# Optimization experiments

Hardware: AMD Instinct MI355X
Metric: run time of the kernel (lower is better)

## Reference

```python
import jax, jax.numpy as jnp
import numpy as np

N_LAYERS = 2        # f_aux_layer_num
DIM = 512           # aux_dim
HEADS = 8           # aux_attn_num
HEAD = DIM // HEADS # 64 == aux_attn_dim
FFN_H = int(DIM * 2.0)  # ffn_factor = 2.0 -> 1024
BLOCK = 64          # f_block_size n
L_BLOCKS = 32
M = BLOCK + 1       # block + router token
EPS = 1e-5
THETA = 10000.0


def rms_norm(x, w):
    return x * jax.lax.rsqrt(jnp.mean(x * x, axis=-1, keepdims=True) + EPS) * w


def rotary(x):
    # x: [b, h, s, a]; matches RotaryEmb: halves rotated with outer(t, inv_freq)
    s, a = x.shape[2], x.shape[3]
    inv_freq = (1.0 / THETA) ** (jnp.arange(0, a, 2, dtype=jnp.float32) / a)
    freqs = jnp.arange(s, dtype=jnp.float32)[:, None] * inv_freq[None, :]  # [s, a/2]
    cos, sin = jnp.cos(freqs), jnp.sin(freqs)
    x1, x2 = jnp.split(x, 2, axis=-1)
    return jnp.concatenate([x1 * cos + x2 * sin, -x1 * sin + x2 * cos], axis=-1)


def setup_inputs() -> dict:
    key = jax.random.key(0)
    ks = jax.random.split(key, 10)
    B = 2
    S = L_BLOCKS * M
    x = jax.random.normal(ks[0], (B, L_BLOCKS * BLOCK, DIM), jnp.float32)
    doc = jnp.sort(jax.random.randint(ks[1], (B, S), 0, 4, dtype=jnp.int32), axis=-1)
    w = 0.02
    return {
        "x": x,
        "doc": doc,
        "router_token": jax.random.normal(ks[2], (DIM,), jnp.float32),
        "attn_w": jax.random.normal(ks[3], (N_LAYERS, DIM, 3 * DIM), jnp.float32) * w,
        "attn_o_w": jax.random.normal(ks[4], (N_LAYERS, DIM, DIM), jnp.float32) * w,
        "ffn_up_w": jax.random.normal(ks[5], (N_LAYERS, DIM, 2 * FFN_H), jnp.float32) * w,
        "ffn_down_w": jax.random.normal(ks[6], (N_LAYERS, FFN_H, DIM), jnp.float32) * w,
        "attn_norm_w": jnp.ones((N_LAYERS, DIM), jnp.float32),
        "ffn_norm_w": jnp.ones((N_LAYERS, DIM), jnp.float32),
    }


def reference(x, doc, router_token, attn_w, attn_o_w, ffn_up_w, ffn_down_w,
              attn_norm_w, ffn_norm_w):
    b = x.shape[0]
    # insert router token after each block: [b, l, n+1, d] -> [b, s, d]
    xb = x.reshape(b, L_BLOCKS, BLOCK, DIM)
    rt = jnp.broadcast_to(router_token, (b, L_BLOCKS, 1, DIM))
    h = jnp.concatenate([xb, rt], axis=2).reshape(b, L_BLOCKS * M, DIM)
    s = h.shape[1]

    # mask_mod_1: block-causal AND same-doc
    blk = jnp.arange(s) // M
    causal = blk[:, None] >= blk[None, :]                       # [s, s]
    mask = causal[None] & (doc[:, :, None] == doc[:, None, :])  # [b, s, s]
    neg = jnp.finfo(h.dtype).min
    scale = 1.0 / jnp.sqrt(jnp.float32(HEAD))

    def split_heads(t):
        return t.reshape(b, s, HEADS, HEAD).transpose(0, 2, 1, 3)

    for i in range(N_LAYERS):
        hn = rms_norm(h, attn_norm_w[i])
        qkv = hn @ attn_w[i]                       # [b, s, 3*dim]
        q, k, v = jnp.split(qkv, 3, axis=-1)
        q, k, v = split_heads(q), split_heads(k), split_heads(v)
        q, k = rotary(q), rotary(k)
        scores = jnp.einsum('bhqa,bhka->bhqk', q, k) * scale
        scores = jnp.where(mask[:, None], scores, neg)
        attn = jax.nn.softmax(scores, axis=-1)
        o = jnp.einsum('bhqk,bhka->bhqa', attn, v)
        o = o.transpose(0, 2, 1, 3).reshape(b, s, DIM)
        h = h + o @ attn_o_w[i]
        hf = rms_norm(h, ffn_norm_w[i])
        u1, u2 = jnp.split(hf @ ffn_up_w[i], 2, axis=-1)
        h = h + (jax.nn.silu(u1) * u2) @ ffn_down_w[i]

    # keep router-token slot of each block: [b, l, d]
    return h.reshape(b, L_BLOCKS, M, DIM)[:, :, -1]
```

## Files before the change

kernel.cpp:

```cpp
#include <hip/hip_runtime.h>
#include <math.h>

#define NB 2
#define LB 32
#define BLKN 64
#define MM 65
#define SS (LB*MM)
#define DD 512
#define NH 8
#define HD 64
#define FFH 1024
#define ROWS (NB*SS)
#define WT_LS 2621440

typedef __attribute__((ext_vector_type(8))) short bf16x8;
typedef __attribute__((ext_vector_type(4))) float f32x4;

__device__ __forceinline__ unsigned short f2bf(float f) {
    union { float f; unsigned u; } v; v.f = f;
    unsigned r = (v.u + 0x7FFFu + ((v.u >> 16) & 1u)) >> 16;
    return (unsigned short)r;
}
__device__ __forceinline__ float bf2f(unsigned short u) {
    union { unsigned u; float f; } v; v.u = ((unsigned)u) << 16; return v.f;
}

__device__ __forceinline__ void gload_lds16(const unsigned short* g, unsigned short* l) {
    __builtin_amdgcn_global_load_lds((const __attribute__((address_space(1))) unsigned int*)g,
                                     (__attribute__((address_space(3))) unsigned int*)l,
                                     16, 0, 0);
}

__device__ __forceinline__ int grow_map(int r) {
    return (r >> 5) * SS + (r & 31) * MM + BLKN;
}

template <int FIRST>
__global__ __launch_bounds__(256) void rms4_k(const float* __restrict__ hsrc,
                                              const float* __restrict__ x,
                                              const float* __restrict__ rt,
                                              const float* __restrict__ w,
                                              float* __restrict__ hout,
                                              unsigned short* __restrict__ out) {
    int row = blockIdx.x * 4 + (threadIdx.x >> 6);
    int lane = threadIdx.x & 63;
    const float* sp;
    if (FIRST) {
        int s = row % SS, b = row / SS;
        int l = s / MM, j = s % MM;
        sp = (j < BLKN) ? x + ((size_t)(b * LB + l) * BLKN + j) * DD : rt;
    } else {
        sp = hsrc + (size_t)row * DD;
    }
    float4 a = *(const float4*)(sp + lane * 8);
    float4 bq = *(const float4*)(sp + lane * 8 + 4);
    float ss = a.x * a.x + a.y * a.y + a.z * a.z + a.w * a.w
             + bq.x * bq.x + bq.y * bq.y + bq.z * bq.z + bq.w * bq.w;
    #pragma unroll
    for (int off = 32; off; off >>= 1) ss += __shfl_xor(ss, off);
    float r = rsqrtf(ss * (1.0f / 512.0f) + 1e-5f);
    float4 w0 = *(const float4*)(w + lane * 8);
    float4 w1 = *(const float4*)(w + lane * 8 + 4);
    unsigned short o8[8] = {f2bf(a.x * r * w0.x), f2bf(a.y * r * w0.y),
                            f2bf(a.z * r * w0.z), f2bf(a.w * r * w0.w),
                            f2bf(bq.x * r * w1.x), f2bf(bq.y * r * w1.y),
                            f2bf(bq.z * r * w1.z), f2bf(bq.w * r * w1.w)};
    *(bf16x8*)(out + (size_t)row * DD + lane * 8) = *(const bf16x8*)o8;
    if (FIRST) {
        *(float4*)(hout + (size_t)row * DD + lane * 8) = a;
        *(float4*)(hout + (size_t)row * DD + lane * 8 + 4) = bq;
    }
}

__global__ __launch_bounds__(256) void wtrans_all_k(const float* __restrict__ attn_w,
                                                    const float* __restrict__ attn_o_w,
                                                    const float* __restrict__ up_w,
                                                    const float* __restrict__ down_w,
                                                    unsigned short* __restrict__ wt) {
    __shared__ unsigned short T[64][66];
    int wg = blockIdx.x;
    int layer = wg >= 640;
    int r = wg - layer * 640;
    const float* W; int K, N; size_t dstOff; int perm = 0;
    if (r < 192)      { W = attn_w   + (size_t)layer * 512 * 1536; K = 512;  N = 1536; dstOff = 0; }
    else if (r < 256) { W = attn_o_w + (size_t)layer * 512 * 512;  K = 512;  N = 512;  dstOff = 786432;  r -= 192; }
    else if (r < 512) { W = up_w     + (size_t)layer * 512 * 2048; K = 512;  N = 2048; dstOff = 1048576; perm = 1; r -= 256; }
    else              { W = down_w   + (size_t)layer * 1024 * 512; K = 1024; N = 512;  dstOff = 2097152; r -= 512; }
    unsigned short* dst = wt + (size_t)layer * WT_LS + dstOff;
    int ntn = N >> 6;
    int n0 = (r % ntn) * 64, k0 = (r / ntn) * 64;
    int t = threadIdx.x;
    #pragma unroll
    for (int i = 0; i < 16; ++i) {
        int e = t + i * 256;
        int rr = e >> 6, cc = e & 63;
        T[rr][cc] = f2bf(W[(size_t)(k0 + rr) * N + n0 + cc]);
    }
    __syncthreads();
    #pragma unroll
    for (int i = 0; i < 16; ++i) {
        int e = t + i * 256;
        int rr = e >> 6, cc = e & 63;
        int n = n0 + rr;
        int nr = n;
        if (perm) {
            int p = n & 1023;
            nr = ((p >> 4) << 5) | ((n >> 10) << 4) | (p & 15);
        }
        dst[(size_t)nr * K + k0 + cc] = T[cc][rr];
    }
}

template <int ADD, int OBF, int ROPE, int SILU>
__global__ __launch_bounds__(256) void gemm128_k(const unsigned short* __restrict__ A,
                                                 const unsigned short* __restrict__ Wt,
                                                 void* __restrict__ Cp,
                                                 int K, int N, int colOff) {
    __shared__ unsigned short As[128 * 64];
    __shared__ unsigned short Bs[128 * 64];
    int t = threadIdx.x;
    int lane = t & 63, wv = t >> 6;
    int wm = wv >> 1, wn = wv & 1;
    int rowBase = blockIdx.y * 128, colBase = blockIdx.x * 128;
    int c = lane & 15, g = lane >> 4;
    int sw = (c & 7) << 4;

    f32x4 acc[4][4];
    #pragma unroll
    for (int mt = 0; mt < 4; ++mt)
        #pragma unroll
        for (int nt = 0; nt < 4; ++nt) { f32x4 z = {0, 0, 0, 0}; acc[mt][nt] = z; }

    for (int k0 = 0; k0 < K; k0 += 64) {
        __syncthreads();
        #pragma unroll
        for (int i = 0; i < 4; ++i) {
            int e0 = (i * 4 + wv) * 64;
            int e = e0 + lane;
            int row = e >> 3;
            int kb = ((e & 7) << 4) ^ ((row & 7) << 4);
            int gr = rowBase + row; if (gr > ROWS - 1) gr = ROWS - 1;
            gload_lds16(A + (size_t)gr * K + k0 + (kb >> 1), &As[e0 * 8]);
        }
        #pragma unroll
        for (int i = 0; i < 4; ++i) {
            int e0 = (i * 4 + wv) * 64;
            int e = e0 + lane;
            int row = e >> 3;
            int kb = ((e & 7) << 4) ^ ((row & 7) << 4);
            gload_lds16(Wt + (size_t)(colOff + colBase + row) * K + k0 + (kb >> 1), &Bs[e0 * 8]);
        }
        __syncthreads();

        bf16x8 af[4][2], bfr[4][2];
        #pragma unroll
        for (int mt = 0; mt < 4; ++mt)
            #pragma unroll
            for (int hf = 0; hf < 2; ++hf)
                af[mt][hf] = *(const bf16x8*)
                    &As[((wm * 64 + mt * 16 + c) * 128 + ((hf * 64 + g * 16) ^ sw)) >> 1];
        #pragma unroll
        for (int nt = 0; nt < 4; ++nt)
            #pragma unroll
            for (int hf = 0; hf < 2; ++hf)
                bfr[nt][hf] = *(const bf16x8*)
                    &Bs[((wn * 64 + nt * 16 + c) * 128 + ((hf * 64 + g * 16) ^ sw)) >> 1];
        __builtin_amdgcn_s_setprio(1);
        #pragma unroll
        for (int mt = 0; mt < 4; ++mt)
            #pragma unroll
            for (int nt = 0; nt < 4; ++nt) {
                acc[mt][nt] = __builtin_amdgcn_mfma_f32_16x16x32_bf16(af[mt][0], bfr[nt][0], acc[mt][nt], 0, 0, 0);
                acc[mt][nt] = __builtin_amdgcn_mfma_f32_16x16x32_bf16(af[mt][1], bfr[nt][1], acc[mt][nt], 0, 0, 0);
            }
        __builtin_amdgcn_s_setprio(0);
    }

    if (ROPE) {
        int sec = (colOff + colBase + wn * 64) >> 9;
        if (sec < 2) {
            #pragma unroll
            for (int mt = 0; mt < 4; ++mt)
                #pragma unroll
                for (int j = 0; j < 4; ++j) {
                    int row = rowBase + wm * 64 + mt * 16 + g * 4 + j;
                    int spos = row % SS;
                    #pragma unroll
                    for (int p = 0; p < 2; ++p) {
                        float jj = (float)(c + p * 16);
                        float inv = exp2f(jj * -0.41524101186092030f);
                        float fr = (float)spos * inv;
                        float sn, cs; __sincosf(fr, &sn, &cs);
                        float a = acc[mt][p][j], bb = acc[mt][p + 2][j];
                        acc[mt][p][j] = a * cs + bb * sn;
                        acc[mt][p + 2][j] = -a * sn + bb * cs;
                    }
                }
        }
    }

    #pragma unroll
    for (int mt = 0; mt < 4; ++mt)
        #pragma unroll
        for (int j = 0; j < 4; ++j) {
            int row = rowBase + wm * 64 + mt * 16 + g * 4 + j;
            if (row >= ROWS) continue;
            if (SILU) {
                unsigned short* gr = (unsigned short*)Cp + (size_t)row * 1024;
                #pragma unroll
                for (int ntp = 0; ntp < 2; ++ntp) {
                    int npr = colBase + wn * 64 + ntp * 32;
                    int p = ((npr >> 5) << 4) + c;
                    float u1 = acc[mt][2 * ntp][j];
                    float u2 = acc[mt][2 * ntp + 1][j];
                    gr[p] = f2bf((u1 / (1.0f + __expf(-u1))) * u2);
                }
            } else {
                size_t off = (size_t)row * N + colOff + colBase + wn * 64 + c;
                if (OBF) {
                    unsigned short* cr = (unsigned short*)Cp + off;
                    #pragma unroll
                    for (int nt = 0; nt < 4; ++nt) cr[nt * 16] = f2bf(acc[mt][nt][j]);
                } else {
                    float* cr = (float*)Cp + off;
                    #pragma unroll
                    for (int nt = 0; nt < 4; ++nt) {
                        if (ADD) cr[nt * 16] += acc[mt][nt][j];
                        else     cr[nt * 16] = acc[mt][nt][j];
                    }
                }
            }
        }
}

template <int MODE, int ADD>
__global__ __launch_bounds__(256) void gemm64_k(const unsigned short* __restrict__ A,
                                                const unsigned short* __restrict__ Wt,
                                                void* __restrict__ Cp,
                                                const float* __restrict__ Hsrc,
                                                float* __restrict__ outp,
                                                int K, int N) {
    __shared__ unsigned short As[64 * 64];
    __shared__ unsigned short Bs[128 * 64];
    int t = threadIdx.x;
    int lane = t & 63, wv = t >> 6;
    int wm = wv >> 1, wn = wv & 1;
    int rowBase = blockIdx.y * 64, colBase = blockIdx.x * 128;
    int c = lane & 15, g = lane >> 4;
    int sw = (c & 7) << 4;

    f32x4 acc[2][4];
    #pragma unroll
    for (int mt = 0; mt < 2; ++mt)
        #pragma unroll
        for (int nt = 0; nt < 4; ++nt) { f32x4 z = {0, 0, 0, 0}; acc[mt][nt] = z; }

    for (int k0 = 0; k0 < K; k0 += 64) {
        __syncthreads();
        #pragma unroll
        for (int i = 0; i < 2; ++i) {
            int e0 = (i * 4 + wv) * 64;
            int e = e0 + lane;
            int row = e >> 3;
            int kb = ((e & 7) << 4) ^ ((row & 7) << 4);
            int gr = rowBase + row;
            if (MODE == 1) gr = grow_map(gr);
            gload_lds16(A + (size_t)gr * K + k0 + (kb >> 1), &As[e0 * 8]);
        }
        #pragma unroll
        for (int i = 0; i < 4; ++i) {
            int e0 = (i * 4 + wv) * 64;
            int e = e0 + lane;
            int row = e >> 3;
            int kb = ((e & 7) << 4) ^ ((row & 7) << 4);
            gload_lds16(Wt + (size_t)(colBase + row) * K + k0 + (kb >> 1), &Bs[e0 * 8]);
        }
        __syncthreads();

        bf16x8 af[2][2], bfr[4][2];
        #pragma unroll
        for (int mt = 0; mt < 2; ++mt)
            #pragma unroll
            for (int hf = 0; hf < 2; ++hf)
                af[mt][hf] = *(const bf16x8*)
                    &As[((wm * 32 + mt * 16 + c) * 128 + ((hf * 64 + g * 16) ^ sw)) >> 1];
        #pragma unroll
        for (int nt = 0; nt < 4; ++nt)
            #pragma unroll
            for (int hf = 0; hf < 2; ++hf)
                bfr[nt][hf] = *(const bf16x8*)
                    &Bs[((wn * 64 + nt * 16 + c) * 128 + ((hf * 64 + g * 16) ^ sw)) >> 1];
        __builtin_amdgcn_s_setprio(1);
        #pragma unroll
        for (int mt = 0; mt < 2; ++mt)
            #pragma unroll
            for (int nt = 0; nt < 4; ++nt) {
                acc[mt][nt] = __builtin_amdgcn_mfma_f32_16x16x32_bf16(af[mt][0], bfr[nt][0], acc[mt][nt], 0, 0, 0);
                acc[mt][nt] = __builtin_amdgcn_mfma_f32_16x16x32_bf16(af[mt][1], bfr[nt][1], acc[mt][nt], 0, 0, 0);
            }
        __builtin_amdgcn_s_setprio(0);
    }

    #pragma unroll
    for (int mt = 0; mt < 2; ++mt)
        #pragma unroll
        for (int j = 0; j < 4; ++j) {
            int row = rowBase + wm * 32 + mt * 16 + g * 4 + j;
            int col = colBase + wn * 64 + c;
            if (MODE == 0) {
                float* cr = (float*)Cp + (size_t)row * N + col;
                #pragma unroll
                for (int nt = 0; nt < 4; ++nt) {
                    if (ADD) cr[nt * 16] += acc[mt][nt][j];
                    else     cr[nt * 16] = acc[mt][nt][j];
                }
            } else if (MODE == 1) {
                int gr = grow_map(row);
                int spos = gr % SS;
                #pragma unroll
                for (int p = 0; p < 2; ++p) {
                    float jj = (float)(c + p * 16);
                    float inv = exp2f(jj * -0.41524101186092030f);
                    float fr = (float)spos * inv;
                    float sn, cs; __sincosf(fr, &sn, &cs);
                    float a = acc[mt][p][j], bb = acc[mt][p + 2][j];
                    acc[mt][p][j] = a * cs + bb * sn;
                    acc[mt][p + 2][j] = -a * sn + bb * cs;
                }
                unsigned short* cr = (unsigned short*)Cp + (size_t)gr * 1536 + col;
                #pragma unroll
                for (int nt = 0; nt < 4; ++nt) cr[nt * 16] = f2bf(acc[mt][nt][j]);
            } else if (MODE == 2) {
                int gr = grow_map(row);
                float* cr = (float*)Cp + (size_t)row * 512 + col;
                const float* hsr = Hsrc + (size_t)gr * 512 + col;
                #pragma unroll
                for (int nt = 0; nt < 4; ++nt) cr[nt * 16] = hsr[nt * 16] + acc[mt][nt][j];
            } else if (MODE == 3) {
                float* cr = outp + (size_t)row * 512 + col;
                const float* hsr = Hsrc + (size_t)row * 512 + col;
                #pragma unroll
                for (int nt = 0; nt < 4; ++nt) cr[nt * 16] = hsr[nt * 16] + acc[mt][nt][j];
            } else {
                unsigned short* gr = (unsigned short*)Cp + (size_t)row * 1024;
                #pragma unroll
                for (int ntp = 0; ntp < 2; ++ntp) {
                    int npr = colBase + wn * 64 + ntp * 32;
                    int p = ((npr >> 5) << 4) + c;
                    float u1 = acc[mt][2 * ntp][j];
                    float u2 = acc[mt][2 * ntp + 1][j];
                    gr[p] = f2bf((u1 / (1.0f + __expf(-u1))) * u2);
                }
            }
        }
}

#define QR 80

template <int ROUTER>
__global__ __launch_bounds__(320) void attn_mfma_k(const unsigned short* __restrict__ qkv,
                                                   const int* __restrict__ doc,
                                                   unsigned short* __restrict__ o,
                                                   unsigned short* __restrict__ obr) {
    __shared__ unsigned short Qs[QR * 64];
    __shared__ unsigned short Ks[2][64 * 64];
    __shared__ unsigned short Vt[2][64][72];
    __shared__ unsigned short Ps[5][16][72];
    __shared__ int docq[QR];
    __shared__ int dock[2][64];

    int idx = blockIdx.x;
    int l = 31 - (idx >> 4);
    int b = (idx >> 3) & 1;
    int h = idx & 7;
    int t = threadIdx.x;
    int lane = t & 63;
    int wv = t >> 6;

    const unsigned short* qb = qkv + (size_t)b * SS * 1536;
    int rowq0 = l * MM;
    int kmax = (l + 1) * MM;

    #pragma unroll
    for (int it = 0; it < 2; ++it) {
        int ebase = it * 320 + wv * 64;
        int e = ebase + lane;
        int row = e >> 3;
        int kb = ((e & 7) << 4) ^ ((row & 7) << 4);
        int gr = rowq0 + row; if (gr > SS - 1) gr = SS - 1;
        gload_lds16(qb + (size_t)gr * 1536 + h * 64 + (kb >> 1), &Qs[ebase * 8]);
    }
    if (t < QR) docq[t] = (t < MM) ? doc[b * SS + rowq0 + t] : -999999;

    int d0 = doc[b * SS + rowq0 + (ROUTER ? BLKN : 0)];
    int lo = 0, hi = rowq0;
    while (lo < hi) {
        int mid = (lo + hi) >> 1;
        if (doc[b * SS + mid] < d0) lo = mid + 1; else hi = mid;
    }
    int kts = lo >> 6;
    int nkt = (kmax + 63) >> 6;

    const int mt = wv;
    const int g = lane >> 4;
    const int c = lane & 15;
    const int sw = (c & 7) << 4;
    const bool act = ROUTER ? (wv == 4) : true;

    auto stageK = [&](int kbase, int buf) {
        int ebase = wv * 64;
        int e = ebase + lane;
        int row = e >> 3;
        int kb = ((e & 7) << 4) ^ ((row & 7) << 4);
        int kg = kbase + row; if (kg > kmax - 1) kg = kmax - 1;
        gload_lds16(qb + (size_t)kg * 1536 + 512 + h * 64 + (kb >> 1), &Ks[buf][ebase * 8]);
        if (wv < 3) {
            int eb2 = 320 + wv * 64;
            int e2 = eb2 + lane;
            int row2 = e2 >> 3;
            int kb2 = ((e2 & 7) << 4) ^ ((row2 & 7) << 4);
            int kg2 = kbase + row2; if (kg2 > kmax - 1) kg2 = kmax - 1;
            gload_lds16(qb + (size_t)kg2 * 1536 + 512 + h * 64 + (kb2 >> 1), &Ks[buf][eb2 * 8]);
        }
    };
    bf16x8 vr0, vr1; int dnx = 0;
    auto loadV = [&](int kbase) {
        int key = t & 63;
        int de = (t >> 6) * 8;
        int kg = kbase + key; if (kg > kmax - 1) kg = kmax - 1;
        vr0 = *(const bf16x8*)(qb + (size_t)kg * 1536 + 1024 + h * 64 + de);
        if (t < 192) {
            int e2 = 320 + t;
            int key2 = e2 & 63;
            int de2 = (e2 >> 6) * 8;
            int kg2 = kbase + key2; if (kg2 > kmax - 1) kg2 = kmax - 1;
            vr1 = *(const bf16x8*)(qb + (size_t)kg2 * 1536 + 1024 + h * 64 + de2);
        }
        if (t < 64) dnx = (kbase + t < kmax) ? doc[b * SS + kbase + t] : -1000000;
    };
    auto writeV = [&](int buf) {
        int key = t & 63;
        int de = (t >> 6) * 8;
        #pragma unroll
        for (int jj = 0; jj < 8; ++jj) Vt[buf][de + jj][key] = ((unsigned short*)&vr0)[jj];
        if (t < 192) {
            int e2 = 320 + t;
            int key2 = e2 & 63;
            int de2 = (e2 >> 6) * 8;
            #pragma unroll
            for (int jj = 0; jj < 8; ++jj) Vt[buf][de2 + jj][key2] = ((unsigned short*)&vr1)[jj];
        }
        if (t < 64) dock[buf][t] = dnx;
    };

    stageK(kts << 6, 0);
    loadV(kts << 6);
    writeV(0);
    __syncthreads();

    bf16x8 aq[2];
    #pragma unroll
    for (int hf = 0; hf < 2; ++hf)
        aq[hf] = *(const bf16x8*)&Qs[((mt * 16 + c) * 128 + ((hf * 64 + g * 16) ^ sw)) >> 1];
    int dq[4];
    #pragma unroll
    for (int j = 0; j < 4; ++j) dq[j] = docq[mt * 16 + g * 4 + j];

    f32x4 oacc[4];
    float m_[4], l_[4];
    #pragma unroll
    for (int nt = 0; nt < 4; ++nt) { f32x4 z = {0,0,0,0}; oacc[nt] = z; }
    #pragma unroll
    for (int j = 0; j < 4; ++j) { m_[j] = -1e30f; l_[j] = 0.0f; }

    for (int kt = kts; kt < nkt; ++kt) {
        int cur = (kt - kts) & 1;
        bool more = (kt + 1 < nkt);
        if (more) {
            stageK((kt + 1) << 6, cur ^ 1);
            loadV((kt + 1) << 6);
        }

        if (act) {
            f32x4 s[4];
            __builtin_amdgcn_s_setprio(1);
            #pragma unroll
            for (int sub = 0; sub < 4; ++sub) {
                f32x4 acc = {0, 0, 0, 0};
                #pragma unroll
                for (int hf = 0; hf < 2; ++hf) {
                    bf16x8 bk = *(const bf16x8*)
                        &Ks[cur][((sub * 16 + c) * 128 + ((hf * 64 + g * 16) ^ sw)) >> 1];
                    acc = __builtin_amdgcn_mfma_f32_16x16x32_bf16(aq[hf], bk, acc, 0, 0, 0);
                }
                s[sub] = acc;
            }
            __builtin_amdgcn_s_setprio(0);
            #pragma unroll
            for (int sub = 0; sub < 4; ++sub) {
                int dk = dock[cur][sub * 16 + c];
                #pragma unroll
                for (int j = 0; j < 4; ++j)
                    s[sub][j] = (dq[j] == dk) ? s[sub][j] * 0.125f : -1e30f;
            }
            float mx[4];
            #pragma unroll
            for (int j = 0; j < 4; ++j)
                mx[j] = fmaxf(fmaxf(s[0][j], s[1][j]), fmaxf(s[2][j], s[3][j]));
            #pragma unroll
            for (int off = 1; off < 16; off <<= 1)
                #pragma unroll
                for (int j = 0; j < 4; ++j) mx[j] = fmaxf(mx[j], __shfl_xor(mx[j], off));
            float mn[4], sc[4], rs[4];
            #pragma unroll
            for (int j = 0; j < 4; ++j) {
                mn[j] = fmaxf(m_[j], mx[j]);
                sc[j] = __expf(m_[j] - mn[j]);
                m_[j] = mn[j];
                rs[j] = 0.0f;
            }
            #pragma unroll
            for (int sub = 0; sub < 4; ++sub)
                #pragma unroll
                for (int j = 0; j < 4; ++j) {
                    float p = __expf(s[sub][j] - mn[j]);
                    rs[j] += p;
                    Ps[wv][g * 4 + j][sub * 16 + c] = f2bf(p);
                }
            #pragma unroll
            for (int off = 1; off < 16; off <<= 1)
                #pragma unroll
                for (int j = 0; j < 4; ++j) rs[j] += __shfl_xor(rs[j], off);
            #pragma unroll
            for (int j = 0; j < 4; ++j) l_[j] = l_[j] * sc[j] + rs[j];
            #pragma unroll
            for (int nt = 0; nt < 4; ++nt)
                #pragma unroll
                for (int j = 0; j < 4; ++j) oacc[nt][j] *= sc[j];
            __builtin_amdgcn_s_setprio(1);
            #pragma unroll
            for (int hf = 0; hf < 2; ++hf) {
                bf16x8 af = *(const bf16x8*)&Ps[wv][c][hf * 32 + g * 8];
                #pragma unroll
                for (int nt = 0; nt < 4; ++nt) {
                    bf16x8 bv = *(const bf16x8*)&Vt[cur][nt * 16 + c][hf * 32 + g * 8];
                    oacc[nt] = __builtin_amdgcn_mfma_f32_16x16x32_bf16(af, bv, oacc[nt], 0, 0, 0);
                }
            }
            __builtin_amdgcn_s_setprio(0);
        }

        if (more) writeV(cur ^ 1);
        __syncthreads();
    }

    if (act) {
        #pragma unroll
        for (int j = 0; j < 4; ++j) {
            int row = mt * 16 + g * 4 + j;
            if (ROUTER) {
                if (row == BLKN) {
                    float invl = 1.0f / l_[j];
                    #pragma unroll
                    for (int nt = 0; nt < 4; ++nt)
                        obr[(size_t)(b * LB + l) * DD + h * 64 + nt * 16 + c] =
                            f2bf(oacc[nt][j] * invl), obr += 0;
                }
            } else if (row < MM) {
                float invl = 1.0f / l_[j];
                #pragma unroll
                for (int nt = 0; nt < 4; ++nt)
                    o[(size_t)(b * SS + rowq0 + row) * DD + h * 64 + nt * 16 + c] =
                        f2bf(oacc[nt][j] * invl);
            }
        }
    }
}

extern "C" void kernel_launch(void* const* d_in, const int* in_sizes, int n_in,
                              void* d_out, int out_size, void* d_ws, size_t ws_size,
                              hipStream_t stream) {
    const float* x           = (const float*)d_in[0];
    const int*   doc         = (const int*)d_in[1];
    const float* rt          = (const float*)d_in[2];
    const float* attn_w      = (const float*)d_in[3];
    const float* attn_o_w    = (const float*)d_in[4];
    const float* ffn_up_w    = (const float*)d_in[5];
    const float* ffn_down_w  = (const float*)d_in[6];
    const float* attn_norm_w = (const float*)d_in[7];
    const float* ffn_norm_w  = (const float*)d_in[8];
    float* out = (float*)d_out;

    float* h = (float*)d_ws;
    unsigned short* qkvb = (unsigned short*)(h + (size_t)ROWS * 512);
    unsigned short* wt   = qkvb + (size_t)ROWS * 1536;
    unsigned short* hnb  = wt + (size_t)2 * WT_LS;
    unsigned short* ob   = hnb + (size_t)ROWS * 512;
    unsigned short* gb   = ob + (size_t)ROWS * 512;
    unsigned short* obr  = gb + (size_t)ROWS * 1024;
    unsigned short* hnr  = obr + 64 * 512;
    unsigned short* gbr  = hnr + 64 * 512;
    float* hr = (float*)(gbr + 64 * 1024);

    wtrans_all_k<<<1280, 256, 0, stream>>>(attn_w, attn_o_w, ffn_up_w, ffn_down_w, wt);

    rms4_k<1><<<ROWS / 4, 256, 0, stream>>>(h, x, rt, attn_norm_w, h, hnb);
    gemm128_k<0, 1, 1, 0><<<dim3(12, 33), 256, 0, stream>>>(hnb, wt, qkvb, 512, 1536, 0);
    attn_mfma_k<0><<<512, 320, 0, stream>>>(qkvb, doc, ob, nullptr);
    gemm64_k<0, 1><<<dim3(4, 65), 256, 0, stream>>>(ob, wt + 786432, h, nullptr, nullptr, 512, 512);
    rms4_k<0><<<ROWS / 4, 256, 0, stream>>>(h, x, rt, ffn_norm_w, h, hnb);
    gemm128_k<0, 0, 0, 1><<<dim3(16, 33), 256, 0, stream>>>(hnb, wt + 1048576, gb, 512, 2048, 0);
    gemm64_k<0, 1><<<dim3(4, 65), 256, 0, stream>>>(gb, wt + 2097152, h, nullptr, nullptr, 1024, 512);

    unsigned short* wl = wt + (size_t)WT_LS;
    rms4_k<0><<<ROWS / 4, 256, 0, stream>>>(h, x, rt, attn_norm_w + 512, h, hnb);
    gemm128_k<0, 1, 1, 0><<<dim3(8, 33), 256, 0, stream>>>(hnb, wl, qkvb, 512, 1536, 512);
    gemm64_k<1, 0><<<dim3(4, 1), 256, 0, stream>>>(hnb, wl, qkvb, nullptr, nullptr, 512, 512);
    attn_mfma_k<1><<<512, 320, 0, stream>>>(qkvb, doc, nullptr, obr);
    gemm64_k<2, 0><<<dim3(4, 1), 256, 0, stream>>>(obr, wl + 786432, hr, h, nullptr, 512, 512);
    rms4_k<0><<<16, 256, 0, stream>>>(hr, x, rt, ffn_norm_w + 512, nullptr, hnr);
    gemm64_k<4, 0><<<dim3(16, 1), 256, 0, stream>>>(hnr, wl + 1048576, gbr, nullptr, nullptr, 512, 2048);
    gemm64_k<3, 0><<<dim3(4, 1), 256, 0, stream>>>(gbr, wl + 2097152, nullptr, hr, out, 1024, 512);
}
```

Measured before the change: 205.8 us.

## Fuse router-row Q projection into a dedicated single-query attention kernel

In the last layer only the router-token rows are needed. The separate router-query GEMM and the 320-thread MFMA attention (where only one wave did work) are replaced by a 64-thread kernel. That kernel computes the query projection for one router row and head, applies rotary, and runs scalar softmax attention over the valid key range found by binary search on doc. The goal is to remove a launch and the wasted idle waves and K/V tiling for a single query row. The cost is scalar FMA loops with strided, uncoalesced V reads.

Result: slower. 231.8 us (+12.6%).

```diff
diff --git a/kernel.cpp b/kernel.cpp
--- a/kernel.cpp
+++ b/kernel.cpp
@@ -264,7 +264,6 @@
             int row = e >> 3;
             int kb = ((e & 7) << 4) ^ ((row & 7) << 4);
             int gr = rowBase + row;
-            if (MODE == 1) gr = grow_map(gr);
             gload_lds16(A + (size_t)gr * K + k0 + (kb >> 1), &As[e0 * 8]);
         }
         #pragma unroll
@@ -314,22 +313,6 @@
                     if (ADD) cr[nt * 16] += acc[mt][nt][j];
                     else     cr[nt * 16] = acc[mt][nt][j];
                 }
-            } else if (MODE == 1) {
-                int gr = grow_map(row);
-                int spos = gr % SS;
-                #pragma unroll
-                for (int p = 0; p < 2; ++p) {
-                    float jj = (float)(c + p * 16);
-                    float inv = exp2f(jj * -0.41524101186092030f);
-                    float fr = (float)spos * inv;
-                    float sn, cs; __sincosf(fr, &sn, &cs);
-                    float a = acc[mt][p][j], bb = acc[mt][p + 2][j];
-                    acc[mt][p][j] = a * cs + bb * sn;
-                    acc[mt][p + 2][j] = -a * sn + bb * cs;
-                }
-                unsigned short* cr = (unsigned short*)Cp + (size_t)gr * 1536 + col;
-                #pragma unroll
-                for (int nt = 0; nt < 4; ++nt) cr[nt * 16] = f2bf(acc[mt][nt][j]);
             } else if (MODE == 2) {
                 int gr = grow_map(row);
                 float* cr = (float*)Cp + (size_t)row * 512 + col;
@@ -357,11 +340,9 @@
 
 #define QR 80
 
-template <int ROUTER>
 __global__ __launch_bounds__(320) void attn_mfma_k(const unsigned short* __restrict__ qkv,
                                                    const int* __restrict__ doc,
-                                                   unsigned short* __restrict__ o,
-                                                   unsigned short* __restrict__ obr) {
+                                                   unsigned short* __restrict__ o) {
     __shared__ unsigned short Qs[QR * 64];
     __shared__ unsigned short Ks[2][64 * 64];
     __shared__ unsigned short Vt[2][64][72];
@@ -392,7 +373,7 @@
     }
     if (t < QR) docq[t] = (t < MM) ? doc[b * SS + rowq0 + t] : -999999;
 
-    int d0 = doc[b * SS + rowq0 + (ROUTER ? BLKN : 0)];
+    int d0 = doc[b * SS + rowq0];
     int lo = 0, hi = rowq0;
     while (lo < hi) {
         int mid = (lo + hi) >> 1;
@@ -405,7 +386,6 @@
     const int g = lane >> 4;
     const int c = lane & 15;
     const int sw = (c & 7) << 4;
-    const bool act = ROUTER ? (wv == 4) : true;
 
     auto stageK = [&](int kbase, int buf) {
         int ebase = wv * 64;
@@ -481,100 +461,179 @@
             loadV((kt + 1) << 6);
         }
 
-        if (act) {
-            f32x4 s[4];
-            __builtin_amdgcn_s_setprio(1);
-            #pragma unroll
-            for (int sub = 0; sub < 4; ++sub) {
-                f32x4 acc = {0, 0, 0, 0};
-                #pragma unroll
-                for (int hf = 0; hf < 2; ++hf) {
-                    bf16x8 bk = *(const bf16x8*)
-                        &Ks[cur][((sub * 16 + c) * 128 + ((hf * 64 + g * 16) ^ sw)) >> 1];
-                    acc = __builtin_amdgcn_mfma_f32_16x16x32_bf16(aq[hf], bk, acc, 0, 0, 0);
-                }
-                s[sub] = acc;
+        f32x4 s[4];
+        __builtin_amdgcn_s_setprio(1);
+        #pragma unroll
+        for (int sub = 0; sub < 4; ++sub) {
+            f32x4 acc = {0, 0, 0, 0};
+            #pragma unroll
+            for (int hf = 0; hf < 2; ++hf) {
+                bf16x8 bk = *(const bf16x8*)
+                    &Ks[cur][((sub * 16 + c) * 128 + ((hf * 64 + g * 16) ^ sw)) >> 1];
+                acc = __builtin_amdgcn_mfma_f32_16x16x32_bf16(aq[hf], bk, acc, 0, 0, 0);
             }
-            __builtin_amdgcn_s_setprio(0);
-            #pragma unroll
-            for (int sub = 0; sub < 4; ++sub) {
-                int dk = dock[cur][sub * 16 + c];
-                #pragma unroll
-                for (int j = 0; j < 4; ++j)
-                    s[sub][j] = (dq[j] == dk) ? s[sub][j] * 0.125f : -1e30f;
+            s[sub] = acc;
+        }
+        __builtin_amdgcn_s_setprio(0);
+        #pragma unroll
+        for (int sub = 0; sub < 4; ++sub) {
+            int dk = dock[cur][sub * 16 + c];
+            #pragma unroll
+            for (int j = 0; j < 4; ++j)
+                s[sub][j] = (dq[j] == dk) ? s[sub][j] * 0.125f : -1e30f;
+        }
+        float mx[4];
+        #pragma unroll
+        for (int j = 0; j < 4; ++j)
+            mx[j] = fmaxf(fmaxf(s[0][j], s[1][j]), fmaxf(s[2][j], s[3][j]));
+        #pragma unroll
+        for (int off = 1; off < 16; off <<= 1)
+            #pragma unroll
+            for (int j = 0; j < 4; ++j) mx[j] = fmaxf(mx[j], __shfl_xor(mx[j], off));
+        float mn[4], sc[4], rs[4];
+        #pragma unroll
+        for (int j = 0; j < 4; ++j) {
+            mn[j] = fmaxf(m_[j], mx[j]);
+            sc[j] = __expf(m_[j] - mn[j]);
+            m_[j] = mn[j];
+            rs[j] = 0.0f;
+        }
+        #pragma unroll
+        for (int sub = 0; sub < 4; ++sub)
+            #pragma unroll
+            for (int j = 0; j < 4; ++j) {
+                float p = __expf(s[sub][j] - mn[j]);
+                rs[j] += p;
+                Ps[wv][g * 4 + j][sub * 16 + c] = f2bf(p);
             }
-            float mx[4];
-            #pragma unroll
-            for (int j = 0; j < 4; ++j)
-                mx[j] = fmaxf(fmaxf(s[0][j], s[1][j]), fmaxf(s[2][j], s[3][j]));
-            #pragma unroll
-            for (int off = 1; off < 16; off <<= 1)
-                #pragma unroll
-                for (int j = 0; j < 4; ++j) mx[j] = fmaxf(mx[j], __shfl_xor(mx[j], off));
-            float mn[4], sc[4], rs[4];
-            #pragma unroll
-            for (int j = 0; j < 4; ++j) {
-                mn[j] = fmaxf(m_[j], mx[j]);
-                sc[j] = __expf(m_[j] - mn[j]);
-                m_[j] = mn[j];
-                rs[j] = 0.0f;
+        #pragma unroll
+        for (int off = 1; off < 16; off <<= 1)
+            #pragma unroll
+            for (int j = 0; j < 4; ++j) rs[j] += __shfl_xor(rs[j], off);
+        #pragma unroll
+        for (int j = 0; j < 4; ++j) l_[j] = l_[j] * sc[j] + rs[j];
+        #pragma unroll
+        for (int nt = 0; nt < 4; ++nt)
+            #pragma unroll
+            for (int j = 0; j < 4; ++j) oacc[nt][j] *= sc[j];
+        __builtin_amdgcn_s_setprio(1);
+        #pragma unroll
+        for (int hf = 0; hf < 2; ++hf) {
+            bf16x8 af = *(const bf16x8*)&Ps[wv][c][hf * 32 + g * 8];
+            #pragma unroll
+            for (int nt = 0; nt < 4; ++nt) {
+                bf16x8 bv = *(const bf16x8*)&Vt[cur][nt * 16 + c][hf * 32 + g * 8];
+                oacc[nt] = __builtin_amdgcn_mfma_f32_16x16x32_bf16(af, bv, oacc[nt], 0, 0, 0);
             }
-            #pragma unroll
-            for (int sub = 0; sub < 4; ++sub)
-                #pragma unroll
-                for (int j = 0; j < 4; ++j) {
-                    float p = __expf(s[sub][j] - mn[j]);
-                    rs[j] += p;
-                    Ps[wv][g * 4 + j][sub * 16 + c] = f2bf(p);
-                }
-            #pragma unroll
-            for (int off = 1; off < 16; off <<= 1)
-                #pragma unroll
-                for (int j = 0; j < 4; ++j) rs[j] += __shfl_xor(rs[j], off);
-            #pragma unroll
-            for (int j = 0; j < 4; ++j) l_[j] = l_[j] * sc[j] + rs[j];
-            #pragma unroll
-            for (int nt = 0; nt < 4; ++nt)
-                #pragma unroll
-                for (int j = 0; j < 4; ++j) oacc[nt][j] *= sc[j];
-            __builtin_amdgcn_s_setprio(1);
-            #pragma unroll
-            for (int hf = 0; hf < 2; ++hf) {
-                bf16x8 af = *(const bf16x8*)&Ps[wv][c][hf * 32 + g * 8];
-                #pragma unroll
-                for (int nt = 0; nt < 4; ++nt) {
-                    bf16x8 bv = *(const bf16x8*)&Vt[cur][nt * 16 + c][hf * 32 + g * 8];
-                    oacc[nt] = __builtin_amdgcn_mfma_f32_16x16x32_bf16(af, bv, oacc[nt], 0, 0, 0);
-                }
-            }
-            __builtin_amdgcn_s_setprio(0);
-        }
+        }
+        __builtin_amdgcn_s_setprio(0);
 
         if (more) writeV(cur ^ 1);
         __syncthreads();
     }
 
-    if (act) {
-        #pragma unroll
-        for (int j = 0; j < 4; ++j) {
-            int row = mt * 16 + g * 4 + j;
-            if (ROUTER) {
-                if (row == BLKN) {
-                    float invl = 1.0f / l_[j];
-                    #pragma unroll
-                    for (int nt = 0; nt < 4; ++nt)
-                        obr[(size_t)(b * LB + l) * DD + h * 64 + nt * 16 + c] =
-                            f2bf(oacc[nt][j] * invl), obr += 0;
-                }
-            } else if (row < MM) {
-                float invl = 1.0f / l_[j];
-                #pragma unroll
-                for (int nt = 0; nt < 4; ++nt)
-                    o[(size_t)(b * SS + rowq0 + row) * DD + h * 64 + nt * 16 + c] =
-                        f2bf(oacc[nt][j] * invl);
-            }
-        }
-    }
+    #pragma unroll
+    for (int j = 0; j < 4; ++j) {
+        int row = mt * 16 + g * 4 + j;
+        if (row < MM) {
+            float invl = 1.0f / l_[j];
+            #pragma unroll
+            for (int nt = 0; nt < 4; ++nt)
+                o[(size_t)(b * SS + rowq0 + row) * DD + h * 64 + nt * 16 + c] =
+                    f2bf(oacc[nt][j] * invl);
+        }
+    }
+}
+
+__global__ __launch_bounds__(64) void rattn_k(const unsigned short* __restrict__ hnb,
+                                              const unsigned short* __restrict__ qkv,
+                                              const unsigned short* __restrict__ wq,
+                                              const int* __restrict__ doc,
+                                              unsigned short* __restrict__ obr) {
+    __shared__ float hn_r[DD];
+    __shared__ float qs[HD];
+    __shared__ float sc[SS];
+
+    int idx = blockIdx.x;
+    int b = idx >> 8, h = (idx >> 5) & 7, l = idx & 31;
+    int lane = threadIdx.x;
+
+    const unsigned short* qb = qkv + (size_t)b * SS * 1536;
+    int spos = l * MM + BLKN;
+    int rowq = b * SS + spos;
+    int kmax = (l + 1) * MM;
+
+    {
+        bf16x8 v8 = *(const bf16x8*)(hnb + (size_t)rowq * DD + lane * 8);
+        #pragma unroll
+        for (int j = 0; j < 8; ++j) hn_r[lane * 8 + j] = bf2f((unsigned short)v8[j]);
+    }
+    int dr = doc[rowq];
+    int lo = 0, hi = spos;
+    while (lo < hi) {
+        int mid = (lo + hi) >> 1;
+        if (doc[b * SS + mid] < dr) lo = mid + 1; else hi = mid;
+    }
+    __syncthreads();
+
+    float dot = 0.0f;
+    {
+        const unsigned short* wr = wq + (size_t)(h * 64 + lane) * DD;
+        #pragma unroll
+        for (int k8 = 0; k8 < 64; ++k8) {
+            bf16x8 w8 = *(const bf16x8*)(wr + k8 * 8);
+            #pragma unroll
+            for (int j = 0; j < 8; ++j)
+                dot += hn_r[k8 * 8 + j] * bf2f((unsigned short)w8[j]);
+        }
+    }
+    {
+        float other = __shfl_xor(dot, 32);
+        float jj = (float)(lane & 31);
+        float inv = exp2f(jj * -0.41524101186092030f);
+        float fr = (float)spos * inv;
+        float sn, cs; __sincosf(fr, &sn, &cs);
+        float q1 = (lane < 32) ? dot : other;
+        float q2 = (lane < 32) ? other : dot;
+        qs[lane] = (lane < 32) ? (q1 * cs + q2 * sn) : (-q1 * sn + q2 * cs);
+    }
+    __syncthreads();
+
+    float mx = -1e30f;
+    for (int k = lo + lane; k < kmax; k += 64) {
+        const unsigned short* kr = qb + (size_t)k * 1536 + 512 + h * 64;
+        float d = 0.0f;
+        #pragma unroll
+        for (int d8 = 0; d8 < 8; ++d8) {
+            bf16x8 k8 = *(const bf16x8*)(kr + d8 * 8);
+            #pragma unroll
+            for (int j = 0; j < 8; ++j)
+                d += bf2f((unsigned short)k8[j]) * qs[d8 * 8 + j];
+        }
+        float s = d * 0.125f;
+        sc[k] = s;
+        mx = fmaxf(mx, s);
+    }
+    #pragma unroll
+    for (int off = 32; off; off >>= 1) mx = fmaxf(mx, __shfl_xor(mx, off));
+    float sum = 0.0f;
+    for (int k = lo + lane; k < kmax; k += 64) {
+        float p = __expf(sc[k] - mx);
+        sc[k] = p;
+        sum += p;
+    }
+    #pragma unroll
+    for (int off = 32; off; off >>= 1) sum += __shfl_xor(sum, off);
+    __syncthreads();
+
+    float inv_l = 1.0f / sum;
+    float acc = 0.0f;
+    #pragma unroll 4
+    for (int k = lo; k < kmax; ++k) {
+        float vv = bf2f(qb[(size_t)k * 1536 + 1024 + h * 64 + lane]);
+        acc += sc[k] * vv;
+    }
+    obr[(size_t)(b * LB + l) * DD + h * 64 + lane] = f2bf(acc * inv_l);
 }
 
 extern "C" void kernel_launch(void* const* d_in, const int* in_sizes, int n_in,
@@ -606,7 +665,7 @@
 
     rms4_k<1><<<ROWS / 4, 256, 0, stream>>>(h, x, rt, attn_norm_w, h, hnb);
     gemm128_k<0, 1, 1, 0><<<dim3(12, 33), 256, 0, stream>>>(hnb, wt, qkvb, 512, 1536, 0);
-    attn_mfma_k<0><<<512, 320, 0, stream>>>(qkvb, doc, ob, nullptr);
+    attn_mfma_k<<<512, 320, 0, stream>>>(qkvb, doc, ob);
     gemm64_k<0, 1><<<dim3(4, 65), 256, 0, stream>>>(ob, wt + 786432, h, nullptr, nullptr, 512, 512);
     rms4_k<0><<<ROWS / 4, 256, 0, stream>>>(h, x, rt, ffn_norm_w, h, hnb);
     gemm128_k<0, 0, 0, 1><<<dim3(16, 33), 256, 0, stream>>>(hnb, wt + 1048576, gb, 512, 2048, 0);
@@ -615,8 +674,7 @@
     unsigned short* wl = wt + (size_t)WT_LS;
     rms4_k<0><<<ROWS / 4, 256, 0, stream>>>(h, x, rt, attn_norm_w + 512, h, hnb);
     gemm128_k<0, 1, 1, 0><<<dim3(8, 33), 256, 0, stream>>>(hnb, wl, qkvb, 512, 1536, 512);
-    gemm64_k<1, 0><<<dim3(4, 1), 256, 0, stream>>>(hnb, wl, qkvb, nullptr, nullptr, 512, 512);
-    attn_mfma_k<1><<<512, 320, 0, stream>>>(qkvb, doc, nullptr, obr);
+    rattn_k<<<512, 64, 0, stream>>>(hnb, qkvb, wl, doc, obr);
     gemm64_k<2, 0><<<dim3(4, 1), 256, 0, stream>>>(obr, wl + 786432, hr, h, nullptr, 512, 512);
     rms4_k<0><<<16, 256, 0, stream>>>(hr, x, rt, ffn_norm_w + 512, nullptr, hnr);
     gemm64_k<4, 0><<<dim3(16, 1), 256, 0, stream>>>(hnr, wl + 1048576, gbr, nullptr, nullptr, 512, 2048);
```
